# Optimization experiments

Hardware: AMD Instinct MI355X
Metric: run time of the kernel (lower is better)

Reference implementation:

```python
import jax, jax.numpy as jnp
import numpy as np

N = 10000
E = 320000
C = 16


def gcn_conv(x, edge_index, W, b, num_nodes):
    # PyG GCNConv: h = X W, then symmetric-normalized aggregation with self-loops, then + b
    h = x @ W  # [N, F_out]
    loop = jnp.arange(num_nodes, dtype=edge_index.dtype)
    src = jnp.concatenate([edge_index[0], loop])
    dst = jnp.concatenate([edge_index[1], loop])
    ones = jnp.ones(src.shape[0], dtype=h.dtype)
    deg = jax.ops.segment_sum(ones, dst, num_segments=num_nodes)  # in-degree incl. self-loop
    dinv = jnp.where(deg > 0, jax.lax.rsqrt(deg), 0.0)
    norm = dinv[src] * dinv[dst]  # [E+N]
    msg = h[src] * norm[:, None]  # gather + scale
    out = jax.ops.segment_sum(msg, dst, num_segments=num_nodes)  # scatter-add
    return out + b


def setup_inputs() -> dict:
    key = jax.random.key(0)
    ks = jax.random.split(key, 8)
    x = jax.random.normal(ks[0], (N, N), dtype=jnp.float32)
    edge_index = jax.random.randint(ks[1], (2, E), 0, N, dtype=jnp.int64)
    W1 = jax.random.normal(ks[2], (N, 64), dtype=jnp.float32) * (1.0 / np.sqrt(N))
    b1 = jnp.zeros((64,), dtype=jnp.float32)
    W2 = jax.random.normal(ks[3], (64, 64), dtype=jnp.float32) * (1.0 / 8.0)
    b2 = jnp.zeros((64,), dtype=jnp.float32)
    W3 = jax.random.normal(ks[4], (64, C), dtype=jnp.float32) * (1.0 / 8.0)
    b3 = jnp.zeros((C,), dtype=jnp.float32)
    return {"x": x, "edge_index": edge_index, "W1": W1, "b1": b1,
            "W2": W2, "b2": b2, "W3": W3, "b3": b3}


def reference(x, edge_index, W1, b1, W2, b2, W3, b3):
    h = jax.nn.relu(gcn_conv(x, edge_index, W1, b1, N))
    h = jax.nn.relu(gcn_conv(h, edge_index, W2, b2, N))
    h = gcn_conv(h, edge_index, W3, b3, N)
    return jax.nn.softmax(h, axis=1)
```

## Files before the change

kernel.cpp:

```cpp
#include <hip/hip_runtime.h>

#define N_NODES 10000
#define E_EDGES 320000


__global__ void k_hist(const int* __restrict__ dst, int* __restrict__ deg) {
    int e = blockIdx.x * blockDim.x + threadIdx.x;
    if (e < E_EDGES) atomicAdd(&deg[dst[e]], 1);
}

__global__ void k_dinv(const int* __restrict__ deg, float* __restrict__ dinv) {
    int i = blockIdx.x * blockDim.x + threadIdx.x;
    if (i < N_NODES) dinv[i] = rsqrtf(1.0f + (float)deg[i]);
}

__global__ void k_scan(const int* __restrict__ deg, int* __restrict__ roff) {
    __shared__ int sums[256];
    __shared__ int offs[256];
    const int CH = 40;
    int t = threadIdx.x;
    int base = t * CH;
    int s = 0;
    for (int i = 0; i < CH; i++) {
        int idx = base + i;
        if (idx < N_NODES) s += deg[idx];
    }
    sums[t] = s;
    __syncthreads();
    if (t == 0) {
        int r = 0;
        for (int i = 0; i < 256; i++) { offs[i] = r; r += sums[i]; }
    }
    __syncthreads();
    int r = offs[t];
    for (int i = 0; i < CH; i++) {
        int idx = base + i;
        if (idx < N_NODES) { roff[idx] = r; r += deg[idx]; }
    }
    if (t == 255) roff[N_NODES] = E_EDGES;
}

__global__ void k_scatter(const int* __restrict__ src, const int* __restrict__ dst,
                          const int* __restrict__ roff, int* __restrict__ cursor,
                          const float* __restrict__ dinv,
                          int* __restrict__ csrc, float* __restrict__ cw) {
    int e = blockIdx.x * blockDim.x + threadIdx.x;
    if (e >= E_EDGES) return;
    int s = src[e], d = dst[e];
    int slot = roff[d] + atomicAdd(&cursor[d], 1);
    csrc[slot] = s;
    cw[slot] = dinv[s] * dinv[d];
}


#define G1_BM 128
#define G1_BK 32
#define G1_CHUNK 1280

__global__ void k_gemm1(const float* __restrict__ x, const float* __restrict__ W1,
                        float* __restrict__ out) {
    __shared__ float As[G1_BK][G1_BM + 4];
    __shared__ float Bs[G1_BK][64];
    int tid = threadIdx.x;
    int tx = tid & 15;
    int ty = tid >> 4;
    int m0 = blockIdx.x * G1_BM;
    int ks = blockIdx.y * G1_CHUNK;
    int ke = min(ks + G1_CHUNK, N_NODES);
    float acc[8][4] = {};

    for (int k0 = ks; k0 < ke; k0 += G1_BK) {
        for (int f = tid; f < 1024; f += 256) {
            int row = f >> 3;
            int kq = f & 7;
            int gm = m0 + row, gk = k0 + kq * 4;
            float4 v = make_float4(0.f, 0.f, 0.f, 0.f);
            if (gm < N_NODES && gk < ke)
                v = *(const float4*)(x + (long)gm * N_NODES + gk);
            As[kq * 4 + 0][row] = v.x;
            As[kq * 4 + 1][row] = v.y;
            As[kq * 4 + 2][row] = v.z;
            As[kq * 4 + 3][row] = v.w;
        }
        for (int f = tid; f < 512; f += 256) {
            int kk = f >> 4, cq = f & 15;
            int gk = k0 + kk;
            float4 v = make_float4(0.f, 0.f, 0.f, 0.f);
            if (gk < ke) v = *(const float4*)(W1 + (long)gk * 64 + cq * 4);
            *(float4*)&Bs[kk][cq * 4] = v;
        }
        __syncthreads();

        for (int kk = 0; kk < G1_BK; kk++) {
            float4 b4 = *(const float4*)&Bs[kk][tx * 4];
            float4 a0 = *(const float4*)&As[kk][ty * 8];
            float4 a1 = *(const float4*)&As[kk][ty * 8 + 4];
            float ar[8] = {a0.x, a0.y, a0.z, a0.w, a1.x, a1.y, a1.z, a1.w};
            float br[4] = {b4.x, b4.y, b4.z, b4.w};
#pragma unroll
            for (int i = 0; i < 8; i++)
#pragma unroll
                for (int j = 0; j < 4; j++)
                    acc[i][j] = fmaf(ar[i], br[j], acc[i][j]);
        }
        __syncthreads();
    }

#pragma unroll
    for (int i = 0; i < 8; i++) {
        int gm = m0 + ty * 8 + i;
        if (gm < N_NODES) {
            float* o = out + gm * 64 + tx * 4;
            atomicAdd(o + 0, acc[i][0]);
            atomicAdd(o + 1, acc[i][1]);
            atomicAdd(o + 2, acc[i][2]);
            atomicAdd(o + 3, acc[i][3]);
        }
    }
}


__global__ void k_gemm64(const float* __restrict__ in, const float* __restrict__ W,
                         float* __restrict__ out) {
    __shared__ float Ws[64 * 64];
    __shared__ float Ain[4][64];
    int tid = threadIdx.x;
    int tx = tid & 63, ty = tid >> 6;
    for (int f = tid; f < 1024; f += 256)
        *(float4*)&Ws[f * 4] = *(const float4*)&W[f * 4];
    int gm = blockIdx.x * 4 + ty;
    Ain[ty][tx] = in[gm * 64 + tx];
    __syncthreads();
    float acc = 0.f;
#pragma unroll
    for (int k = 0; k < 64; k++) acc = fmaf(Ain[ty][k], Ws[k * 64 + tx], acc);
    out[gm * 64 + tx] = acc;
}

__global__ void k_gemm16(const float* __restrict__ in, const float* __restrict__ W,
                         float* __restrict__ out) {
    __shared__ float Ws[64 * 16];
    __shared__ float Ain[16][64];
    int tid = threadIdx.x;
    int tx = tid & 15, ty = tid >> 4;
    *(float4*)&Ws[tid * 4] = *(const float4*)&W[tid * 4];
    {
        int r = tid >> 4, kq = tid & 15;
        *(float4*)&Ain[r][kq * 4] =
            *(const float4*)(in + (long)(blockIdx.x * 16 + r) * 64 + kq * 4);
    }
    __syncthreads();
    float acc = 0.f;
#pragma unroll
    for (int k = 0; k < 64; k++) acc = fmaf(Ain[ty][k], Ws[k * 16 + tx], acc);
    out[(blockIdx.x * 16 + ty) * 16 + tx] = acc;
}


__global__ void k_agg64(const float* __restrict__ h, const float* __restrict__ bias,
                        const int* __restrict__ roff, const int* __restrict__ csrc,
                        const float* __restrict__ cw, const float* __restrict__ dinv,
                        float* __restrict__ out, int do_relu) {
    int n = blockIdx.x * 4 + (threadIdx.x >> 6);
    int c = threadIdx.x & 63;
    float di = dinv[n];
    float acc = di * di * h[n * 64 + c];
    int e0 = roff[n], e1 = roff[n + 1];
    for (int e = e0; e < e1; e++)
        acc = fmaf(cw[e], h[csrc[e] * 64 + c], acc);
    acc += bias[c];
    if (do_relu) acc = fmaxf(acc, 0.f);
    out[n * 64 + c] = acc;
}

__global__ void k_agg16_softmax(const float* __restrict__ h, const float* __restrict__ b3,
                                const int* __restrict__ roff, const int* __restrict__ csrc,
                                const float* __restrict__ cw, const float* __restrict__ dinv,
                                float* __restrict__ out) {
    int lane = threadIdx.x & 63;
    int n = blockIdx.x * 4 + (threadIdx.x >> 6);
    int c = lane & 15, g = lane >> 4;
    float di = dinv[n];
    float acc = (g == 0) ? di * di * h[n * 16 + c] : 0.f;
    int e0 = roff[n], e1 = roff[n + 1];
    for (int e = e0 + g; e < e1; e += 4)
        acc = fmaf(cw[e], h[csrc[e] * 16 + c], acc);
    acc += __shfl_xor(acc, 16);
    acc += __shfl_xor(acc, 32);
    float logit = acc + b3[c];
    float m = logit;
    m = fmaxf(m, __shfl_xor(m, 1));
    m = fmaxf(m, __shfl_xor(m, 2));
    m = fmaxf(m, __shfl_xor(m, 4));
    m = fmaxf(m, __shfl_xor(m, 8));
    float ex = expf(logit - m);
    float s = ex;
    s += __shfl_xor(s, 1);
    s += __shfl_xor(s, 2);
    s += __shfl_xor(s, 4);
    s += __shfl_xor(s, 8);
    if (g == 0) out[n * 16 + c] = ex / s;
}


extern "C" void kernel_launch(void* const* d_in, const int* in_sizes, int n_in,
                              void* d_out, int out_size, void* d_ws, size_t ws_size,
                              hipStream_t stream) {
    (void)in_sizes; (void)n_in; (void)out_size; (void)ws_size;
    const float* x  = (const float*)d_in[0];
    const int*   ei = (const int*)d_in[1];
    const float* W1 = (const float*)d_in[2];
    const float* b1 = (const float*)d_in[3];
    const float* W2 = (const float*)d_in[4];
    const float* b2 = (const float*)d_in[5];
    const float* W3 = (const float*)d_in[6];
    const float* b3 = (const float*)d_in[7];
    float* out = (float*)d_out;
    const int* esrc = ei;
    const int* edst = ei + E_EDGES;

    char* p = (char*)d_ws;
    size_t off = 0;
    auto alloc = [&](size_t b) -> void* {
        void* r = p + off;
        off += (b + 255) & ~(size_t)255;
        return r;
    };
    int*   deg    = (int*)alloc(N_NODES * 4);
    int*   cursor = (int*)alloc(N_NODES * 4);
    int*   roff   = (int*)alloc((N_NODES + 1) * 4);
    float* dinv   = (float*)alloc(N_NODES * 4);
    int*   csrc   = (int*)alloc(E_EDGES * 4);
    float* cw     = (float*)alloc(E_EDGES * 4);
    float* bufA   = (float*)alloc(N_NODES * 64 * 4);
    float* bufB   = (float*)alloc(N_NODES * 64 * 4);
    float* bufC   = (float*)alloc(N_NODES * 16 * 4);

    hipMemsetAsync(deg, 0, N_NODES * 4, stream);
    hipMemsetAsync(cursor, 0, N_NODES * 4, stream);
    hipMemsetAsync(bufA, 0, N_NODES * 64 * 4, stream);

    k_hist<<<(E_EDGES + 255) / 256, 256, 0, stream>>>(edst, deg);
    k_dinv<<<(N_NODES + 255) / 256, 256, 0, stream>>>(deg, dinv);
    k_scan<<<1, 256, 0, stream>>>(deg, roff);
    k_scatter<<<(E_EDGES + 255) / 256, 256, 0, stream>>>(esrc, edst, roff, cursor, dinv,
                                                         csrc, cw);

    k_gemm1<<<dim3((N_NODES + G1_BM - 1) / G1_BM, 8), 256, 0, stream>>>(x, W1, bufA);
    k_agg64<<<N_NODES / 4, 256, 0, stream>>>(bufA, b1, roff, csrc, cw, dinv, bufB, 1);
    k_gemm64<<<N_NODES / 4, 256, 0, stream>>>(bufB, W2, bufA);
    k_agg64<<<N_NODES / 4, 256, 0, stream>>>(bufA, b2, roff, csrc, cw, dinv, bufB, 1);
    k_gemm16<<<N_NODES / 16, 256, 0, stream>>>(bufB, W3, bufC);
    k_agg16_softmax<<<N_NODES / 4, 256, 0, stream>>>(bufC, b3, roff, csrc, cw, dinv, out);
}
```

Before: 855.9 us.

## Use split-bf16 MFMA for first-layer GEMM and unroll aggregation loop

Replaces the fp32 FMA tiled GEMM for X·W1 with an MFMA bf16 kernel that splits each fp32 operand into high and low bf16 parts and issues three MFMAs per tile to approximate fp32 accuracy. W1 is pre-split and transposed into padded bf16 buffers by a new kernel on every call. The aggregation loop is also unrolled by four to expose more independent gathers. The main cost targeted is the compute of the 10000x10000x64 GEMM, which dominates runtime. The trade-off is slightly reduced precision, an extra conversion pass over W1, and in-kernel conversion of x.

```diff
diff --git a/kernel.cpp b/kernel.cpp
--- a/kernel.cpp
+++ b/kernel.cpp
@@ -2,6 +2,19 @@
 
 #define N_NODES 10000
 #define E_EDGES 320000
+#define KP 10016
+
+typedef float f32x4 __attribute__((ext_vector_type(4)));
+typedef __bf16 bf16x8 __attribute__((ext_vector_type(8)));
+
+static __device__ __forceinline__ ushort f2bf(float f) {
+    unsigned u = __float_as_uint(f);
+    unsigned r = (u + 0x7fffu + ((u >> 16) & 1u)) >> 16;
+    return (ushort)r;
+}
+static __device__ __forceinline__ float bf2f(ushort h) {
+    return __uint_as_float(((unsigned)h) << 16);
+}
 
 
 __global__ void k_hist(const int* __restrict__ dst, int* __restrict__ deg) {
@@ -53,70 +66,98 @@
 }
 
 
+__global__ void k_wsplit(const float* __restrict__ W1, ushort* __restrict__ Whi,
+                         ushort* __restrict__ Wlo) {
+    int k = blockIdx.x * 256 + threadIdx.x;
+    int n = blockIdx.y;
+    if (k >= KP) return;
+    ushort h = 0, l = 0;
+    if (k < N_NODES) {
+        float f = W1[(long)k * 64 + n];
+        h = f2bf(f);
+        l = f2bf(f - bf2f(h));
+    }
+    Whi[(long)n * KP + k] = h;
+    Wlo[(long)n * KP + k] = l;
+}
+
+
 #define G1_BM 128
-#define G1_BK 32
 #define G1_CHUNK 1280
 
-__global__ void k_gemm1(const float* __restrict__ x, const float* __restrict__ W1,
-                        float* __restrict__ out) {
-    __shared__ float As[G1_BK][G1_BM + 4];
-    __shared__ float Bs[G1_BK][64];
+__global__ __launch_bounds__(256) void k_gemm1_mfma(
+        const float* __restrict__ x, const ushort* __restrict__ Whi,
+        const ushort* __restrict__ Wlo, float* __restrict__ out) {
+    __shared__ ushort As[2][G1_BM][40];
+    __shared__ ushort Bs[2][64][40];
+
     int tid = threadIdx.x;
-    int tx = tid & 15;
-    int ty = tid >> 4;
+    int lane = tid & 63, wv = tid >> 6;
+    int quad = lane >> 4, lm = lane & 15;
+    int q8 = quad * 8;
     int m0 = blockIdx.x * G1_BM;
     int ks = blockIdx.y * G1_CHUNK;
     int ke = min(ks + G1_CHUNK, N_NODES);
-    float acc[8][4] = {};
-
-    for (int k0 = ks; k0 < ke; k0 += G1_BK) {
-        for (int f = tid; f < 1024; f += 256) {
-            int row = f >> 3;
-            int kq = f & 7;
+
+    f32x4 acc[2][4] = {};
+
+    int bn = tid >> 2, bp = (tid & 3) * 8;
+
+    for (int k0 = ks; k0 < ke; k0 += 32) {
+#pragma unroll
+        for (int i = 0; i < 4; i++) {
+            int f = tid + i * 256;
+            int row = f >> 3, kq = f & 7;
             int gm = m0 + row, gk = k0 + kq * 4;
             float4 v = make_float4(0.f, 0.f, 0.f, 0.f);
-            if (gm < N_NODES && gk < ke)
+            if (gm < N_NODES && gk < N_NODES)
                 v = *(const float4*)(x + (long)gm * N_NODES + gk);
-            As[kq * 4 + 0][row] = v.x;
-            As[kq * 4 + 1][row] = v.y;
-            As[kq * 4 + 2][row] = v.z;
-            As[kq * 4 + 3][row] = v.w;
+            ushort h0 = f2bf(v.x), h1 = f2bf(v.y), h2 = f2bf(v.z), h3 = f2bf(v.w);
+            ushort l0 = f2bf(v.x - bf2f(h0)), l1 = f2bf(v.y - bf2f(h1));
+            ushort l2 = f2bf(v.z - bf2f(h2)), l3 = f2bf(v.w - bf2f(h3));
+            *(ushort4*)&As[0][row][kq * 4] = make_ushort4(h0, h1, h2, h3);
+            *(ushort4*)&As[1][row][kq * 4] = make_ushort4(l0, l1, l2, l3);
         }
-        for (int f = tid; f < 512; f += 256) {
-            int kk = f >> 4, cq = f & 15;
-            int gk = k0 + kk;
-            float4 v = make_float4(0.f, 0.f, 0.f, 0.f);
-            if (gk < ke) v = *(const float4*)(W1 + (long)gk * 64 + cq * 4);
-            *(float4*)&Bs[kk][cq * 4] = v;
+        *(float4*)&Bs[0][bn][bp] = *(const float4*)&Whi[(long)bn * KP + k0 + bp];
+        *(float4*)&Bs[1][bn][bp] = *(const float4*)&Wlo[(long)bn * KP + k0 + bp];
+        __syncthreads();
+
+        bf16x8 ah[2], al[2], bh[4], bl[4];
+#pragma unroll
+        for (int r = 0; r < 2; r++) {
+            int row = wv * 32 + r * 16 + lm;
+            ah[r] = *(const bf16x8*)&As[0][row][q8];
+            al[r] = *(const bf16x8*)&As[1][row][q8];
         }
+#pragma unroll
+        for (int c = 0; c < 4; c++) {
+            int n = c * 16 + lm;
+            bh[c] = *(const bf16x8*)&Bs[0][n][q8];
+            bl[c] = *(const bf16x8*)&Bs[1][n][q8];
+        }
+#pragma unroll
+        for (int r = 0; r < 2; r++)
+#pragma unroll
+            for (int c = 0; c < 4; c++) {
+                acc[r][c] = __builtin_amdgcn_mfma_f32_16x16x32_bf16(al[r], bh[c], acc[r][c], 0, 0, 0);
+                acc[r][c] = __builtin_amdgcn_mfma_f32_16x16x32_bf16(ah[r], bl[c], acc[r][c], 0, 0, 0);
+                acc[r][c] = __builtin_amdgcn_mfma_f32_16x16x32_bf16(ah[r], bh[c], acc[r][c], 0, 0, 0);
+            }
         __syncthreads();
-
-        for (int kk = 0; kk < G1_BK; kk++) {
-            float4 b4 = *(const float4*)&Bs[kk][tx * 4];
-            float4 a0 = *(const float4*)&As[kk][ty * 8];
-            float4 a1 = *(const float4*)&As[kk][ty * 8 + 4];
-            float ar[8] = {a0.x, a0.y, a0.z, a0.w, a1.x, a1.y, a1.z, a1.w};
-            float br[4] = {b4.x, b4.y, b4.z, b4.w};
-#pragma unroll
-            for (int i = 0; i < 8; i++)
-#pragma unroll
-                for (int j = 0; j < 4; j++)
-                    acc[i][j] = fmaf(ar[i], br[j], acc[i][j]);
+    }
+
+#pragma unroll
+    for (int r = 0; r < 2; r++)
+#pragma unroll
+        for (int c = 0; c < 4; c++) {
+            int row0 = m0 + wv * 32 + r * 16 + quad * 4;
+            int cn = c * 16 + lm;
+#pragma unroll
+            for (int i = 0; i < 4; i++) {
+                int gm = row0 + i;
+                if (gm < N_NODES) atomicAdd(&out[gm * 64 + cn], acc[r][c][i]);
+            }
         }
-        __syncthreads();
-    }
-
-#pragma unroll
-    for (int i = 0; i < 8; i++) {
-        int gm = m0 + ty * 8 + i;
-        if (gm < N_NODES) {
-            float* o = out + gm * 64 + tx * 4;
-            atomicAdd(o + 0, acc[i][0]);
-            atomicAdd(o + 1, acc[i][1]);
-            atomicAdd(o + 2, acc[i][2]);
-            atomicAdd(o + 3, acc[i][3]);
-        }
-    }
 }
 
 
@@ -166,7 +207,18 @@
     float di = dinv[n];
     float acc = di * di * h[n * 64 + c];
     int e0 = roff[n], e1 = roff[n + 1];
-    for (int e = e0; e < e1; e++)
+    int e = e0;
+    for (; e + 3 < e1; e += 4) {
+        int s0 = csrc[e], s1 = csrc[e + 1], s2 = csrc[e + 2], s3 = csrc[e + 3];
+        float w0 = cw[e], w1 = cw[e + 1], w2 = cw[e + 2], w3 = cw[e + 3];
+        float v0 = h[s0 * 64 + c], v1 = h[s1 * 64 + c];
+        float v2 = h[s2 * 64 + c], v3 = h[s3 * 64 + c];
+        acc = fmaf(w0, v0, acc);
+        acc = fmaf(w1, v1, acc);
+        acc = fmaf(w2, v2, acc);
+        acc = fmaf(w3, v3, acc);
+    }
+    for (; e < e1; e++)
         acc = fmaf(cw[e], h[csrc[e] * 64 + c], acc);
     acc += bias[c];
     if (do_relu) acc = fmaxf(acc, 0.f);
@@ -226,15 +278,17 @@
         off += (b + 255) & ~(size_t)255;
         return r;
     };
-    int*   deg    = (int*)alloc(N_NODES * 4);
-    int*   cursor = (int*)alloc(N_NODES * 4);
-    int*   roff   = (int*)alloc((N_NODES + 1) * 4);
-    float* dinv   = (float*)alloc(N_NODES * 4);
-    int*   csrc   = (int*)alloc(E_EDGES * 4);
-    float* cw     = (float*)alloc(E_EDGES * 4);
-    float* bufA   = (float*)alloc(N_NODES * 64 * 4);
-    float* bufB   = (float*)alloc(N_NODES * 64 * 4);
-    float* bufC   = (float*)alloc(N_NODES * 16 * 4);
+    int*    deg    = (int*)alloc(N_NODES * 4);
+    int*    cursor = (int*)alloc(N_NODES * 4);
+    int*    roff   = (int*)alloc((N_NODES + 1) * 4);
+    float*  dinv   = (float*)alloc(N_NODES * 4);
+    int*    csrc   = (int*)alloc(E_EDGES * 4);
+    float*  cw     = (float*)alloc(E_EDGES * 4);
+    float*  bufA   = (float*)alloc(N_NODES * 64 * 4);
+    float*  bufB   = (float*)alloc(N_NODES * 64 * 4);
+    float*  bufC   = (float*)alloc(N_NODES * 16 * 4);
+    ushort* Whi    = (ushort*)alloc((size_t)64 * KP * 2);
+    ushort* Wlo    = (ushort*)alloc((size_t)64 * KP * 2);
 
     hipMemsetAsync(deg, 0, N_NODES * 4, stream);
     hipMemsetAsync(cursor, 0, N_NODES * 4, stream);
@@ -245,8 +299,9 @@
     k_scan<<<1, 256, 0, stream>>>(deg, roff);
     k_scatter<<<(E_EDGES + 255) / 256, 256, 0, stream>>>(esrc, edst, roff, cursor, dinv,
                                                          csrc, cw);
-
-    k_gemm1<<<dim3((N_NODES + G1_BM - 1) / G1_BM, 8), 256, 0, stream>>>(x, W1, bufA);
+    k_wsplit<<<dim3((KP + 255) / 256, 64), 256, 0, stream>>>(W1, Whi, Wlo);
+
+    k_gemm1_mfma<<<dim3((N_NODES + G1_BM - 1) / G1_BM, 8), 256, 0, stream>>>(x, Whi, Wlo, bufA);
     k_agg64<<<N_NODES / 4, 256, 0, stream>>>(bufA, b1, roff, csrc, cw, dinv, bufB, 1);
     k_gemm64<<<N_NODES / 4, 256, 0, stream>>>(bufB, W2, bufA);
     k_agg64<<<N_NODES / 4, 256, 0, stream>>>(bufA, b2, roff, csrc, cw, dinv, bufB, 1);
```

Result: faster. 716.8 us (-16.2%).
